# Performance work log

Measured on AMD Instinct MI355X. Metric: run time of the kernel, lower is better.

Reference implementation:

```python
import jax, jax.numpy as jnp
import numpy as np

N_QUBITS = 6      # 4 data + 2 ancilla
N_DATA = 4
N_LAYERS = 4
N_GROUPS = 8
DIM = 2 ** N_QUBITS  # 64 statevector amplitudes (real: RY + CNOT keep state real)
GN_GROUPS = 32
EPS = 1e-5


def _cnot_ring_perm():
    # CNOT(q, q+1 mod n) ring applied sequentially; compose into one basis permutation.
    n = N_QUBITS
    f = np.arange(DIM)
    for c in range(n):
        t = (c + 1) % n
        cbit = (f >> (n - 1 - c)) & 1
        f = np.where(cbit == 1, f ^ (1 << (n - 1 - t)), f)
    # new_state[f[i]] = old_state[i]  =>  new = old[finv]
    finv = np.empty(DIM, dtype=np.int64)
    finv[f] = np.arange(DIM)
    return jnp.asarray(finv)


def _zsign():
    i = np.arange(DIM)[:, None]
    q = np.arange(N_DATA)[None, :]
    return jnp.asarray(1.0 - 2.0 * ((i >> (N_QUBITS - 1 - q)) & 1), dtype=jnp.float32)


PERM = _cnot_ring_perm()
ZSIGN = _zsign()


def _group_norm(x, gamma, beta):
    B, C, H, W = x.shape
    xg = x.reshape(B, GN_GROUPS, C // GN_GROUPS, H, W)
    mu = xg.mean(axis=(2, 3, 4), keepdims=True)
    var = xg.var(axis=(2, 3, 4), keepdims=True)
    xn = ((xg - mu) * jax.lax.rsqrt(var + EPS)).reshape(B, C, H, W)
    return xn * gamma[None, :, None, None] + beta[None, :, None, None]


def _apply_ry(state, half_angle, q):
    # state: [B,H,W,G,64]; half_angle: [B,H,W,G]; RY = [[c,-s],[s,c]] on qubit q
    pre, post = 2 ** q, 2 ** (N_QUBITS - 1 - q)
    s = state.reshape(state.shape[:-1] + (pre, 2, post))
    c = jnp.cos(half_angle)[..., None, None]
    sn = jnp.sin(half_angle)[..., None, None]
    a0, a1 = s[..., 0, :], s[..., 1, :]
    new = jnp.stack([c * a0 - sn * a1, sn * a0 + c * a1], axis=-2)
    return new.reshape(state.shape)


def _forward(x, emb, gamma, beta, w_in, b_in, theta, w_style, b_style, w_out, b_out):
    B, C, H, W = x.shape
    h = _group_norm(x, gamma, beta)                       # norm0
    emb_a = emb * jax.nn.sigmoid(emb)                     # SiLU(emb)
    # 1x1 projection to per-group data-qubit rotation angles: [B,H,W,G,4]
    ang = jnp.einsum('oc,bchw->bohw', w_in, h) + b_in[None, :, None, None]
    ang = ang.reshape(B, N_GROUPS, N_DATA, H, W).transpose(0, 3, 4, 1, 2)
    # style modulation of circuit parameters: [B,G,L,Q]
    style = (emb_a @ w_style.T + b_style).reshape(B, N_GROUPS, N_LAYERS, N_QUBITS)
    # init |0...0> per pixel per group
    state = jnp.zeros((B, H, W, N_GROUPS, DIM), x.dtype).at[..., 0].set(1.0)
    for l in range(N_LAYERS):
        for q in range(N_QUBITS):
            a = theta[:, l, q][None, None, None, :] + style[:, :, l, q][:, None, None, :]
            if q < N_DATA:                                # data reuploading each layer
                a = a + ang[..., q]
            state = _apply_ry(state, 0.5 * a, q)
        state = state[..., PERM]                          # CNOT ring entangler
    probs = state * state
    meas = probs @ ZSIGN                                  # [B,H,W,G,4] <Z> on data qubits
    meas = meas.transpose(0, 3, 4, 1, 2).reshape(B, N_GROUPS * N_DATA, H, W)
    out = jnp.einsum('oc,bchw->bohw', w_out, meas) + b_out[None, :, None, None]
    return out + x                                        # residual


def setup_inputs() -> dict:
    key = jax.random.key(0)
    ks = jax.random.split(key, 6)
    B, C, H, W, E = 16, 256, 32, 32, 512
    return {
        'x': jax.random.normal(ks[0], (B, C, H, W), jnp.float32),
        'emb': jax.random.normal(ks[1], (B, E), jnp.float32),
        'gamma': jnp.ones((C,), jnp.float32),
        'beta': jnp.zeros((C,), jnp.float32),
        'w_in': jax.random.normal(ks[2], (32, C), jnp.float32) * 0.1,
        'b_in': jnp.zeros((32,), jnp.float32),
        'theta': jax.random.normal(ks[3], (N_GROUPS, N_LAYERS, N_QUBITS), jnp.float32) * 0.5,
        'w_style': jax.random.normal(ks[4], (N_GROUPS * N_LAYERS * N_QUBITS, E), jnp.float32) * 0.02,
        'b_style': jnp.zeros((N_GROUPS * N_LAYERS * N_QUBITS,), jnp.float32),
        'w_out': jax.random.normal(ks[5], (C, 32), jnp.float32) * 0.05,
        'b_out': jnp.zeros((C,), jnp.float32),
    }


def reference(x, emb, gamma, beta, w_in, b_in, theta, w_style, b_style, w_out, b_out):
    return _forward(x, emb, gamma, beta, w_in, b_in, theta, w_style, b_style, w_out, b_out)
```

## Files before the change

kernel.cpp:

```cpp
#include <hip/hip_runtime.h>
#include <math.h>

#define NB 16
#define NC 256
#define NHW 1024
#define NE 512
#define NDQ 4
#define NLQ 4
#define NQB 6
#define QDIM 64
#define PIX 8
#define XPAD 260
#define MSP 12

typedef float v2f __attribute__((ext_vector_type(2)));

constexpr int fwd1(int i) {
    int r = i;
    for (int c = 0; c < NQB; ++c) {
        int t = (c + 1) % NQB;
        if ((r >> (NQB - 1 - c)) & 1) r ^= 1 << (NQB - 1 - t);
    }
    return r;
}
constexpr int fwdl(int s, int l) { for (int i = 0; i < l; ++i) s = fwd1(s); return s; }
constexpr int parity6(int x) { x ^= x >> 4; x ^= x >> 2; x ^= x >> 1; return x & 1; }

struct GateTab { int M[NLQ][NQB]; int V[NLQ][NQB]; int W[NDQ]; };
constexpr GateTab make_tab() {
    GateTab g{};
    for (int l = 0; l < NLQ; ++l)
        for (int q = 0; q < NQB; ++q) {
            int m = 1 << (NQB - 1 - q);
            for (int x = 0; x < QDIM; ++x) if (fwdl(x, l) == m) { g.M[l][q] = x; break; }
            int V = 0;
            for (int t = 0; t < NQB; ++t) V |= ((fwdl(1 << t, l) >> (NQB - 1 - q)) & 1) << t;
            g.V[l][q] = V;
        }
    for (int d = 0; d < NDQ; ++d) {
        int W = 0;
        for (int t = 0; t < NQB; ++t) W |= ((fwdl(1 << t, NLQ) >> (NQB - 1 - d)) & 1) << t;
        g.W[d] = W;
    }
    return g;
}
constexpr GateTab GT = make_tab();

__global__ __launch_bounds__(256) void k_pre(const float* __restrict__ x,
                                             const float* __restrict__ emb,
                                             const float* __restrict__ w_style,
                                             const float* __restrict__ b_style,
                                             const float* __restrict__ theta,
                                             float* __restrict__ mu,
                                             float* __restrict__ rs,
                                             float* __restrict__ A) {
    if (blockIdx.x < 512) {
        int bg = blockIdx.x;
        const float4* xp = (const float4*)(x + (size_t)bg * 8 * NHW);
        float s = 0.f, ss = 0.f;
        for (int i = threadIdx.x; i < 8 * NHW / 4; i += 256) {
            float4 v = xp[i];
            s  += v.x + v.y + v.z + v.w;
            ss += v.x*v.x + v.y*v.y + v.z*v.z + v.w*v.w;
        }
        __shared__ float red0[4], red1[4];
        #pragma unroll
        for (int o = 32; o; o >>= 1) { s += __shfl_down(s, o); ss += __shfl_down(ss, o); }
        int lane = threadIdx.x & 63, w = threadIdx.x >> 6;
        if (lane == 0) { red0[w] = s; red1[w] = ss; }
        __syncthreads();
        if (threadIdx.x == 0) {
            s  = red0[0] + red0[1] + red0[2] + red0[3];
            ss = red1[0] + red1[1] + red1[2] + red1[3];
            float m = s * (1.f / 8192.f);
            float var = ss * (1.f / 8192.f) - m * m;
            mu[bg] = m;
            rs[bg] = rsqrtf(var + 1e-5f);
        }
    } else {
        int b = blockIdx.x - 512;
        __shared__ float es[NE];
        int t = threadIdx.x;
        for (int i = t; i < NE; i += 256) {
            float v = emb[b * NE + i];
            es[i] = v / (1.f + __expf(-v));
        }
        __syncthreads();
        int j0 = t >> 3, sub = t & 7;
        for (int pass = 0; pass < 6; ++pass) {
            int j = pass * 32 + j0;
            const float* wr = w_style + (size_t)j * NE + sub * 64;
            const float* er = es + sub * 64;
            float acc = 0.f;
            #pragma unroll
            for (int i = 0; i < 64; i += 4) {
                float4 w4 = *(const float4*)(wr + i);
                acc = fmaf(w4.x, er[i],   acc);
                acc = fmaf(w4.y, er[i+1], acc);
                acc = fmaf(w4.z, er[i+2], acc);
                acc = fmaf(w4.w, er[i+3], acc);
            }
            acc += __shfl_xor(acc, 1);
            acc += __shfl_xor(acc, 2);
            acc += __shfl_xor(acc, 4);
            if (sub == 0) A[b * 192 + j] = theta[j] + b_style[j] + acc;
        }
    }
}

__global__ __launch_bounds__(128, 2) void k_main(
    const float* __restrict__ x,
    const float* __restrict__ gamma,
    const float* __restrict__ beta,
    const float* __restrict__ w_in,
    const float* __restrict__ b_in,
    const float* __restrict__ A,
    const float* __restrict__ w_out,
    const float* __restrict__ b_out,
    const float* __restrict__ mu,
    const float* __restrict__ rs,
    float* __restrict__ out) {

    __shared__ float xs[PIX * XPAD];
    __shared__ float as_[PIX * 36];
    __shared__ float ms[32 * MSP];

    int blk = blockIdx.x;
    int b = blk >> 7;
    int pbase = (blk & 127) * PIX;
    int t = threadIdx.x;
    int c0 = t >> 1, f4 = (t & 1) * 4;

    float4 xr[4];
    #pragma unroll
    for (int k = 0; k < 4; ++k) {
        int c = c0 + 64 * k;
        xr[k] = *(const float4*)(x + (size_t)(b * NC + c) * NHW + pbase + f4);
    }

    #pragma unroll
    for (int k = 0; k < 4; ++k) {
        int c = c0 + 64 * k;
        int g = b * 32 + (c >> 3);
        float sc = rs[g] * gamma[c];
        float sh = fmaf(-mu[g], sc, beta[c]);
        float4 v = xr[k];
        xs[(f4 + 0) * XPAD + c] = fmaf(v.x, sc, sh);
        xs[(f4 + 1) * XPAD + c] = fmaf(v.y, sc, sh);
        xs[(f4 + 2) * XPAD + c] = fmaf(v.z, sc, sh);
        xs[(f4 + 3) * XPAD + c] = fmaf(v.w, sc, sh);
    }
    __syncthreads();

    {
        int og = t >> 3, p = t & 7;
        int o0 = og * 2;
        const v2f* h2  = (const v2f*)(xs + p * XPAD);
        const v2f* w02 = (const v2f*)(w_in + o0 * NC);
        const v2f* w12 = (const v2f*)(w_in + (o0 + 1) * NC);
        v2f a0 = {0.f, 0.f}, a1 = {0.f, 0.f};
        #pragma unroll 16
        for (int c2 = 0; c2 < NC / 2; ++c2) {
            v2f h = h2[c2];
            a0 = __builtin_elementwise_fma(w02[c2], h, a0);
            a1 = __builtin_elementwise_fma(w12[c2], h, a1);
        }
        as_[p * 36 + o0]     = a0.x + a0.y + b_in[o0];
        as_[p * 36 + o0 + 1] = a1.x + a1.y + b_in[o0 + 1];
    }
    __syncthreads();

    #pragma unroll
    for (int k = 0; k < 4; ++k) {
        int c = c0 + 64 * k;
        float4 v = xr[k];
        xs[(f4 + 0) * XPAD + c] = v.x;
        xs[(f4 + 1) * XPAD + c] = v.y;
        xs[(f4 + 2) * XPAD + c] = v.z;
        xs[(f4 + 3) * XPAD + c] = v.w;
    }

    {
        int cir = t >> 1, sub = t & 1;
        int g = cir >> 3, p = cir & 7;
        float4 angv = *(const float4*)(as_ + p * 36 + g * 4);
        float angp[NDQ] = {angv.x, angv.y, angv.z, angv.w};
        float Ar[24];
        {
            const float4* Ab4 = (const float4*)(A + b * 192 + g * 24);
            #pragma unroll
            for (int j = 0; j < 6; ++j) {
                float4 a4 = Ab4[j];
                Ar[4*j] = a4.x; Ar[4*j+1] = a4.y; Ar[4*j+2] = a4.z; Ar[4*j+3] = a4.w;
            }
        }

        v2f st2[16];
        #pragma unroll
        for (int k = 0; k < 16; ++k) st2[k] = (v2f){0.f, 0.f};
        if (sub == 0) st2[0].x = 1.f;

        #pragma unroll
        for (int l = 0; l < NLQ; ++l) {
            #pragma unroll
            for (int q = 0; q < NQB; ++q) {
                const int M  = GT.M[l][q];
                const int V  = GT.V[l][q];
                const int ML = M & 31;
                const int KD = ML >> 1;
                float a = Ar[l * NQB + q] + (q < NDQ ? angp[q] : 0.f);
                float sn, cs;
                __sincosf(0.5f * a, &sn, &cs);
                float snS = (V & 32) ? (sub ? -sn : sn) : sn;
                v2f cs2 = {cs, cs};
                if (M & 32) {
                    v2f pstl[16];
                    #pragma unroll
                    for (int k = 0; k < 16; ++k) {
                        pstl[k].x = __shfl_xor(st2[k].x, 1);
                        pstl[k].y = __shfl_xor(st2[k].y, 1);
                    }
                    #pragma unroll
                    for (int k = 0; k < 16; ++k) {
                        v2f ov = pstl[k ^ KD];
                        if (M & 1) ov = __builtin_shufflevector(ov, ov, 1, 0);
                        v2f co = { parity6((2*k)     & (V & 31)) ? snS : -snS,
                                   parity6((2*k + 1) & (V & 31)) ? snS : -snS };
                        st2[k] = __builtin_elementwise_fma(co, ov, cs2 * st2[k]);
                    }
                } else {
                    v2f nst[16];
                    #pragma unroll
                    for (int k = 0; k < 16; ++k) {
                        v2f ov = st2[k ^ KD];
                        if (M & 1) ov = __builtin_shufflevector(ov, ov, 1, 0);
                        v2f co = { parity6((2*k)     & (V & 31)) ? snS : -snS,
                                   parity6((2*k + 1) & (V & 31)) ? snS : -snS };
                        nst[k] = __builtin_elementwise_fma(co, ov, cs2 * st2[k]);
                    }
                    #pragma unroll
                    for (int k = 0; k < 16; ++k) st2[k] = nst[k];
                }
            }
        }

        #pragma unroll
        for (int k = 0; k < 16; ++k) st2[k] = st2[k] * st2[k];
        #pragma unroll
        for (int d = 0; d < NDQ; ++d) {
            const int W = GT.W[d];
            v2f acc2 = {0.f, 0.f};
            #pragma unroll
            for (int k = 0; k < 16; ++k) {
                v2f sg = { parity6((2*k)     & (W & 31)) ? -1.f : 1.f,
                           parity6((2*k + 1) & (W & 31)) ? -1.f : 1.f };
                acc2 = __builtin_elementwise_fma(sg, st2[k], acc2);
            }
            float pd = acc2.x + acc2.y;
            if (W & 32) pd = sub ? -pd : pd;
            pd += __shfl_xor(pd, 1);
            if (sub == 0) ms[(g * 4 + d) * MSP + p] = pd;
        }
    }
    __syncthreads();

    {
        int cb = t >> 2, f2 = (t & 3) * 2;
        v2f mreg[32];
        #pragma unroll
        for (int o = 0; o < 32; ++o)
            mreg[o] = *(const v2f*)(ms + o * MSP + f2);
        #pragma unroll
        for (int k = 0; k < 8; ++k) {
            int c = cb + 32 * k;
            const float* wr = w_out + c * 32;
            v2f acc = {0.f, 0.f};
            #pragma unroll
            for (int o4 = 0; o4 < 8; ++o4) {
                float4 w4 = *(const float4*)(wr + o4 * 4);
                acc = __builtin_elementwise_fma((v2f){w4.x, w4.x}, mreg[4*o4],     acc);
                acc = __builtin_elementwise_fma((v2f){w4.y, w4.y}, mreg[4*o4 + 1], acc);
                acc = __builtin_elementwise_fma((v2f){w4.z, w4.z}, mreg[4*o4 + 2], acc);
                acc = __builtin_elementwise_fma((v2f){w4.w, w4.w}, mreg[4*o4 + 3], acc);
            }
            float bo = b_out[c];
            float x0 = xs[(f2 + 0) * XPAD + c];
            float x1 = xs[(f2 + 1) * XPAD + c];
            float2 r = {acc.x + bo + x0, acc.y + bo + x1};
            *(float2*)(out + (size_t)(b * NC + c) * NHW + pbase + f2) = r;
        }
    }
}

extern "C" void kernel_launch(void* const* d_in, const int* in_sizes, int n_in,
                              void* d_out, int out_size, void* d_ws, size_t ws_size,
                              hipStream_t stream) {
    const float* x       = (const float*)d_in[0];
    const float* emb     = (const float*)d_in[1];
    const float* gamma   = (const float*)d_in[2];
    const float* beta    = (const float*)d_in[3];
    const float* w_in    = (const float*)d_in[4];
    const float* b_in    = (const float*)d_in[5];
    const float* theta   = (const float*)d_in[6];
    const float* w_style = (const float*)d_in[7];
    const float* b_style = (const float*)d_in[8];
    const float* w_out   = (const float*)d_in[9];
    const float* b_out   = (const float*)d_in[10];
    float* out = (float*)d_out;

    float* ws = (float*)d_ws;
    float* mu = ws;
    float* rs = ws + 512;
    float* A  = ws + 1024;

    k_pre<<<512 + NB, 256, 0, stream>>>(x, emb, w_style, b_style, theta, mu, rs, A);
    k_main<<<NB * 128, 128, 0, stream>>>(x, gamma, beta, w_in, b_in, A,
                                         w_out, b_out, mu, rs, out);
}
```

Before: 141.1 us.

## Simulate each circuit in one thread with 64-thread blocks and swizzled tiles

The block size drops from 128 to 64 threads, and each thread now holds the full 64-amplitude statevector. This removes the cross-lane shuffles that paired threads needed to split a circuit. The RY gates become in-place butterflies over register pairs. The input projection and output projection loops are re-tiled for wider float4 weight loads, the measurements reuse the angle shared buffer, and block indices are swizzled so adjacent pixel tiles map differently. The trade-offs are higher register pressure, fewer waves per block, and scalar (non-vectorized) output stores.

```diff
diff --git a/kernel.cpp b/kernel.cpp
--- a/kernel.cpp
+++ b/kernel.cpp
@@ -11,7 +11,6 @@
 #define QDIM 64
 #define PIX 8
 #define XPAD 260
-#define MSP 12
 
 typedef float v2f __attribute__((ext_vector_type(2)));
 
@@ -108,7 +107,7 @@
     }
 }
 
-__global__ __launch_bounds__(128, 2) void k_main(
+__global__ __launch_bounds__(64, 2) void k_main(
     const float* __restrict__ x,
     const float* __restrict__ gamma,
     const float* __restrict__ beta,
@@ -123,66 +122,70 @@
 
     __shared__ float xs[PIX * XPAD];
     __shared__ float as_[PIX * 36];
-    __shared__ float ms[32 * MSP];
-
-    int blk = blockIdx.x;
-    int b = blk >> 7;
-    int pbase = (blk & 127) * PIX;
+
+    int i = blockIdx.x;
+    int tile = 2 * (i & 7) + 16 * (i >> 4) + ((i >> 3) & 1);
+    int b = tile >> 7;
+    int pbase = (tile & 127) * PIX;
     int t = threadIdx.x;
-    int c0 = t >> 1, f4 = (t & 1) * 4;
-
-    float4 xr[4];
+
+    int cidx = t >> 1, p4 = (t & 1) * 4;
+    float4 xr[8];
     #pragma unroll
-    for (int k = 0; k < 4; ++k) {
-        int c = c0 + 64 * k;
-        xr[k] = *(const float4*)(x + (size_t)(b * NC + c) * NHW + pbase + f4);
+    for (int k = 0; k < 8; ++k) {
+        int c = cidx + 32 * k;
+        xr[k] = *(const float4*)(x + (size_t)(b * NC + c) * NHW + pbase + p4);
     }
 
     #pragma unroll
-    for (int k = 0; k < 4; ++k) {
-        int c = c0 + 64 * k;
+    for (int k = 0; k < 8; ++k) {
+        int c = cidx + 32 * k;
         int g = b * 32 + (c >> 3);
         float sc = rs[g] * gamma[c];
         float sh = fmaf(-mu[g], sc, beta[c]);
         float4 v = xr[k];
-        xs[(f4 + 0) * XPAD + c] = fmaf(v.x, sc, sh);
-        xs[(f4 + 1) * XPAD + c] = fmaf(v.y, sc, sh);
-        xs[(f4 + 2) * XPAD + c] = fmaf(v.z, sc, sh);
-        xs[(f4 + 3) * XPAD + c] = fmaf(v.w, sc, sh);
+        float* bp = xs + p4 * XPAD + c;
+        bp[0]        = fmaf(v.x, sc, sh);
+        bp[XPAD]     = fmaf(v.y, sc, sh);
+        bp[2 * XPAD] = fmaf(v.z, sc, sh);
+        bp[3 * XPAD] = fmaf(v.w, sc, sh);
     }
     __syncthreads();
 
     {
-        int og = t >> 3, p = t & 7;
-        int o0 = og * 2;
-        const v2f* h2  = (const v2f*)(xs + p * XPAD);
-        const v2f* w02 = (const v2f*)(w_in + o0 * NC);
-        const v2f* w12 = (const v2f*)(w_in + (o0 + 1) * NC);
-        v2f a0 = {0.f, 0.f}, a1 = {0.f, 0.f};
-        #pragma unroll 16
-        for (int c2 = 0; c2 < NC / 2; ++c2) {
-            v2f h = h2[c2];
-            a0 = __builtin_elementwise_fma(w02[c2], h, a0);
-            a1 = __builtin_elementwise_fma(w12[c2], h, a1);
-        }
-        as_[p * 36 + o0]     = a0.x + a0.y + b_in[o0];
-        as_[p * 36 + o0 + 1] = a1.x + a1.y + b_in[o0 + 1];
+        int p = t >> 3, og = t & 7;
+        int o0 = og * 4;
+        const float* hrow = xs + p * XPAD;
+        v2f acc[4] = {{0.f,0.f},{0.f,0.f},{0.f,0.f},{0.f,0.f}};
+        #pragma unroll 8
+        for (int c = 0; c < NC; c += 4) {
+            float4 h = *(const float4*)(hrow + c);
+            v2f hlo = {h.x, h.y}, hhi = {h.z, h.w};
+            #pragma unroll
+            for (int r = 0; r < 4; ++r) {
+                float4 w = *(const float4*)(w_in + (o0 + r) * NC + c);
+                acc[r] = __builtin_elementwise_fma((v2f){w.x, w.y}, hlo, acc[r]);
+                acc[r] = __builtin_elementwise_fma((v2f){w.z, w.w}, hhi, acc[r]);
+            }
+        }
+        float4 bi = *(const float4*)(b_in + o0);
+        float4 r4 = {acc[0].x + acc[0].y + bi.x, acc[1].x + acc[1].y + bi.y,
+                     acc[2].x + acc[2].y + bi.z, acc[3].x + acc[3].y + bi.w};
+        *(float4*)(as_ + p * 36 + o0) = r4;
     }
     __syncthreads();
 
     #pragma unroll
-    for (int k = 0; k < 4; ++k) {
-        int c = c0 + 64 * k;
+    for (int k = 0; k < 8; ++k) {
+        int c = cidx + 32 * k;
         float4 v = xr[k];
-        xs[(f4 + 0) * XPAD + c] = v.x;
-        xs[(f4 + 1) * XPAD + c] = v.y;
-        xs[(f4 + 2) * XPAD + c] = v.z;
-        xs[(f4 + 3) * XPAD + c] = v.w;
-    }
+        float* bp = xs + p4 * XPAD + c;
+        bp[0] = v.x; bp[XPAD] = v.y; bp[2 * XPAD] = v.z; bp[3 * XPAD] = v.w;
+    }
+    __syncthreads();
 
     {
-        int cir = t >> 1, sub = t & 1;
-        int g = cir >> 3, p = cir & 7;
+        int g = t >> 3, p = t & 7;
         float4 angv = *(const float4*)(as_ + p * 36 + g * 4);
         float angp[NDQ] = {angv.x, angv.y, angv.z, angv.w};
         float Ar[24];
@@ -195,99 +198,87 @@
             }
         }
 
-        v2f st2[16];
-        #pragma unroll
-        for (int k = 0; k < 16; ++k) st2[k] = (v2f){0.f, 0.f};
-        if (sub == 0) st2[0].x = 1.f;
+        v2f st2[32];
+        #pragma unroll
+        for (int k = 0; k < 32; ++k) st2[k] = (v2f){0.f, 0.f};
+        st2[0].x = 1.f;
 
         #pragma unroll
         for (int l = 0; l < NLQ; ++l) {
             #pragma unroll
             for (int q = 0; q < NQB; ++q) {
-                const int M  = GT.M[l][q];
-                const int V  = GT.V[l][q];
-                const int ML = M & 31;
-                const int KD = ML >> 1;
+                const int M = GT.M[l][q], V = GT.V[l][q];
+                const int KD = M >> 1, SW = M & 1;
+                int hh = KD; hh |= hh >> 1; hh |= hh >> 2; hh |= hh >> 4;
+                const int HB = hh - (hh >> 1);
                 float a = Ar[l * NQB + q] + (q < NDQ ? angp[q] : 0.f);
                 float sn, cs;
                 __sincosf(0.5f * a, &sn, &cs);
-                float snS = (V & 32) ? (sub ? -sn : sn) : sn;
                 v2f cs2 = {cs, cs};
-                if (M & 32) {
-                    v2f pstl[16];
+                v2f sPP = {sn, sn}, sPM = {sn, -sn}, sMP = {-sn, sn}, sMM = {-sn, -sn};
+                auto COV = [&](int i0) -> v2f {
+                    bool p0 = parity6(i0 & V), p1 = parity6((i0 + 1) & V);
+                    return p0 ? (p1 ? sPP : sPM) : (p1 ? sMP : sMM);
+                };
+                if (KD == 0) {
                     #pragma unroll
-                    for (int k = 0; k < 16; ++k) {
-                        pstl[k].x = __shfl_xor(st2[k].x, 1);
-                        pstl[k].y = __shfl_xor(st2[k].y, 1);
-                    }
-                    #pragma unroll
-                    for (int k = 0; k < 16; ++k) {
-                        v2f ov = pstl[k ^ KD];
-                        if (M & 1) ov = __builtin_shufflevector(ov, ov, 1, 0);
-                        v2f co = { parity6((2*k)     & (V & 31)) ? snS : -snS,
-                                   parity6((2*k + 1) & (V & 31)) ? snS : -snS };
-                        st2[k] = __builtin_elementwise_fma(co, ov, cs2 * st2[k]);
+                    for (int k = 0; k < 32; ++k) {
+                        v2f ov = __builtin_shufflevector(st2[k], st2[k], 1, 0);
+                        st2[k] = __builtin_elementwise_fma(COV(2*k), ov, cs2 * st2[k]);
                     }
                 } else {
-                    v2f nst[16];
                     #pragma unroll
-                    for (int k = 0; k < 16; ++k) {
-                        v2f ov = st2[k ^ KD];
-                        if (M & 1) ov = __builtin_shufflevector(ov, ov, 1, 0);
-                        v2f co = { parity6((2*k)     & (V & 31)) ? snS : -snS,
-                                   parity6((2*k + 1) & (V & 31)) ? snS : -snS };
-                        nst[k] = __builtin_elementwise_fma(co, ov, cs2 * st2[k]);
+                    for (int k = 0; k < 32; ++k) {
+                        if (k & HB) continue;
+                        int kp = k ^ KD;
+                        v2f av = st2[k], bv = st2[kp];
+                        v2f am = SW ? __builtin_shufflevector(av, av, 1, 0) : av;
+                        v2f bm = SW ? __builtin_shufflevector(bv, bv, 1, 0) : bv;
+                        st2[k]  = __builtin_elementwise_fma(COV(2*k),  bm, cs2 * av);
+                        st2[kp] = __builtin_elementwise_fma(COV(2*kp), am, cs2 * bv);
                     }
-                    #pragma unroll
-                    for (int k = 0; k < 16; ++k) st2[k] = nst[k];
                 }
             }
         }
 
         #pragma unroll
-        for (int k = 0; k < 16; ++k) st2[k] = st2[k] * st2[k];
+        for (int k = 0; k < 32; ++k) st2[k] = st2[k] * st2[k];
+        float md[NDQ];
         #pragma unroll
         for (int d = 0; d < NDQ; ++d) {
             const int W = GT.W[d];
-            v2f acc2 = {0.f, 0.f};
-            #pragma unroll
-            for (int k = 0; k < 16; ++k) {
-                v2f sg = { parity6((2*k)     & (W & 31)) ? -1.f : 1.f,
-                           parity6((2*k + 1) & (W & 31)) ? -1.f : 1.f };
-                acc2 = __builtin_elementwise_fma(sg, st2[k], acc2);
-            }
-            float pd = acc2.x + acc2.y;
-            if (W & 32) pd = sub ? -pd : pd;
-            pd += __shfl_xor(pd, 1);
-            if (sub == 0) ms[(g * 4 + d) * MSP + p] = pd;
-        }
+            v2f acc = {0.f, 0.f};
+            #pragma unroll
+            for (int k = 0; k < 32; ++k) {
+                v2f sg = { parity6((2*k)     & W) ? -1.f : 1.f,
+                           parity6((2*k + 1) & W) ? -1.f : 1.f };
+                acc = __builtin_elementwise_fma(sg, st2[k], acc);
+            }
+            md[d] = acc.x + acc.y;
+        }
+        float4 mv = {md[0], md[1], md[2], md[3]};
+        *(float4*)(as_ + p * 36 + g * 4) = mv;
     }
     __syncthreads();
 
     {
-        int cb = t >> 2, f2 = (t & 3) * 2;
-        v2f mreg[32];
-        #pragma unroll
-        for (int o = 0; o < 32; ++o)
-            mreg[o] = *(const v2f*)(ms + o * MSP + f2);
-        #pragma unroll
-        for (int k = 0; k < 8; ++k) {
-            int c = cb + 32 * k;
+        int p = t & 7, cs = t >> 3;
+        float4 m4[8];
+        #pragma unroll
+        for (int j = 0; j < 8; ++j) m4[j] = *(const float4*)(as_ + p * 36 + 4 * j);
+        #pragma unroll 4
+        for (int k = 0; k < 32; ++k) {
+            int c = cs + 8 * k;
             const float* wr = w_out + c * 32;
             v2f acc = {0.f, 0.f};
             #pragma unroll
-            for (int o4 = 0; o4 < 8; ++o4) {
-                float4 w4 = *(const float4*)(wr + o4 * 4);
-                acc = __builtin_elementwise_fma((v2f){w4.x, w4.x}, mreg[4*o4],     acc);
-                acc = __builtin_elementwise_fma((v2f){w4.y, w4.y}, mreg[4*o4 + 1], acc);
-                acc = __builtin_elementwise_fma((v2f){w4.z, w4.z}, mreg[4*o4 + 2], acc);
-                acc = __builtin_elementwise_fma((v2f){w4.w, w4.w}, mreg[4*o4 + 3], acc);
-            }
-            float bo = b_out[c];
-            float x0 = xs[(f2 + 0) * XPAD + c];
-            float x1 = xs[(f2 + 1) * XPAD + c];
-            float2 r = {acc.x + bo + x0, acc.y + bo + x1};
-            *(float2*)(out + (size_t)(b * NC + c) * NHW + pbase + f2) = r;
+            for (int j = 0; j < 8; ++j) {
+                float4 w = *(const float4*)(wr + 4 * j);
+                acc = __builtin_elementwise_fma((v2f){w.x, w.y}, (v2f){m4[j].x, m4[j].y}, acc);
+                acc = __builtin_elementwise_fma((v2f){w.z, w.w}, (v2f){m4[j].z, m4[j].w}, acc);
+            }
+            float pd = acc.x + acc.y + b_out[c] + xs[p * XPAD + c];
+            out[(size_t)(b * NC + c) * NHW + pbase + p] = pd;
         }
     }
 }
@@ -314,6 +305,6 @@
     float* A  = ws + 1024;
 
     k_pre<<<512 + NB, 256, 0, stream>>>(x, emb, w_style, b_style, theta, mu, rs, A);
-    k_main<<<NB * 128, 128, 0, stream>>>(x, gamma, beta, w_in, b_in, A,
-                                         w_out, b_out, mu, rs, out);
-}
+    k_main<<<2048, 64, 0, stream>>>(x, gamma, beta, w_in, b_in, A,
+                                    w_out, b_out, mu, rs, out);
+}
```

Result: slower. 179.8 us (+27.4%).
